# Optimization experiments

Measured on AMD Instinct MI355X. Metric: run time of the kernel, lower is better.

## Reference

```python
import jax, jax.numpy as jnp
import numpy as np

PATCH = 7
PAD = PATCH // 2  # 3


def _to_gray(x):
    # x: [B,3,H,W] -> [B,1,H,W]
    return 0.299 * x[:, 0:1] + 0.587 * x[:, 1:2] + 0.114 * x[:, 2:3]


def _census_transform(x):
    # x: [B,C,H,W] RGB -> grayscale, then 48 shifted binary comparisons.
    if x.shape[1] == 3:
        x = _to_gray(x)
    B, C, H, W = x.shape
    x_pad = jnp.pad(x, ((0, 0), (0, 0), (PAD, PAD), (PAD, PAD)), mode='reflect')
    center = x
    feats = []
    for i in range(PATCH):
        for j in range(PATCH):
            if i == PAD and j == PAD:
                continue
            neighbor = x_pad[:, :, i:i + H, j:j + W]
            feats.append((center > neighbor).astype(x.dtype))
    return jnp.concatenate(feats, axis=1)  # [B,48,H,W]


def setup_inputs() -> dict:
    key = jax.random.key(0)
    k1, k2 = jax.random.split(key)
    B, C, H, W = 8, 3, 512, 512
    pred = jax.random.uniform(k1, (B, C, H, W), dtype=jnp.float32)
    target = jax.random.uniform(k2, (B, C, H, W), dtype=jnp.float32)
    return {"pred": pred, "target": target}


def reference(pred, target):
    pred_census = _census_transform(pred)
    target_census = _census_transform(target)
    return jnp.abs(pred_census - target_census).mean()
```

## Files before the change

kernel.cpp:

```cpp
#include <hip/hip_runtime.h>


#define BATCH 8
#define HH 512
#define WW 512
#define PLANE (HH * WW)
#define TW 64
#define TH 32
#define SCOLS 72
#define HROWS 38
#define KPR 18
#define PITCH 44
#define NT 512
#define LDSZ (SCOLS * PITCH)

__device__ __forceinline__ int refl(int v, int n) {
    return v < 0 ? -v : (v >= n ? 2 * n - 2 - v : v);
}
__device__ __forceinline__ int cbase(int lx) {
    return lx * PITCH + (((lx >> 2) & 7) << 2);
}

__device__ __forceinline__ void load_col10(const float* col, float (&w)[10]) {
    const float4 a = *(const float4*)(col);
    const float4 b = *(const float4*)(col + 4);
    const float2 d = *(const float2*)(col + 8);
    w[0] = a.x; w[1] = a.y; w[2] = a.z; w[3] = a.w;
    w[4] = b.x; w[5] = b.y; w[6] = b.z; w[7] = b.w;
    w[8] = d.x; w[9] = d.y;
}

__global__ __launch_bounds__(NT, 8)
void census_fused(const float* __restrict__ pred,
                  const float* __restrict__ target,
                  float* __restrict__ out) {
    __shared__ __align__(16) float sP[LDSZ];
    __shared__ __align__(16) float sT[LDSZ];

    const int b   = blockIdx.z;
    const int ty0 = blockIdx.y * TH;
    const int tx0 = blockIdx.x * TW;
    const float* __restrict__ pb = pred   + (size_t)b * 3 * PLANE;
    const float* __restrict__ tb = target + (size_t)b * 3 * PLANE;
    const bool fastx = (blockIdx.x >= 1 && blockIdx.x <= 6);

    if (fastx) {
        for (int idx = threadIdx.x; idx < HROWS * KPR; idx += NT) {
            const int hy = idx / KPR;
            const int k  = idx - hy * KPR;
            const int gy  = refl(ty0 + hy - 3, HH);
            const int off = gy * WW + tx0 - 4 + 4 * k;
            const float4 pr = *(const float4*)(pb + off);
            const float4 pg = *(const float4*)(pb + off + PLANE);
            const float4 pc = *(const float4*)(pb + off + 2 * PLANE);
            const float4 tr = *(const float4*)(tb + off);
            const float4 tg = *(const float4*)(tb + off + PLANE);
            const float4 tc = *(const float4*)(tb + off + 2 * PLANE);
            const int lx = 4 * k;
            sP[cbase(lx + 0) + hy] = 0.299f * pr.x + 0.587f * pg.x + 0.114f * pc.x;
            sP[cbase(lx + 1) + hy] = 0.299f * pr.y + 0.587f * pg.y + 0.114f * pc.y;
            sP[cbase(lx + 2) + hy] = 0.299f * pr.z + 0.587f * pg.z + 0.114f * pc.z;
            sP[cbase(lx + 3) + hy] = 0.299f * pr.w + 0.587f * pg.w + 0.114f * pc.w;
            sT[cbase(lx + 0) + hy] = 0.299f * tr.x + 0.587f * tg.x + 0.114f * tc.x;
            sT[cbase(lx + 1) + hy] = 0.299f * tr.y + 0.587f * tg.y + 0.114f * tc.y;
            sT[cbase(lx + 2) + hy] = 0.299f * tr.z + 0.587f * tg.z + 0.114f * tc.z;
            sT[cbase(lx + 3) + hy] = 0.299f * tr.w + 0.587f * tg.w + 0.114f * tc.w;
        }
    } else {
        for (int idx = threadIdx.x; idx < HROWS * SCOLS; idx += NT) {
            const int hy = idx / SCOLS;
            const int lx = idx - hy * SCOLS;
            const int gy  = refl(ty0 + hy - 3, HH);
            const int gx  = refl(tx0 + lx - 4, WW);
            const int off = gy * WW + gx;
            sP[cbase(lx) + hy] = 0.299f * pb[off] + 0.587f * pb[off + PLANE] + 0.114f * pb[off + 2 * PLANE];
            sT[cbase(lx) + hy] = 0.299f * tb[off] + 0.587f * tb[off + PLANE] + 0.114f * tb[off + 2 * PLANE];
        }
    }
    __syncthreads();

    const int wv  = threadIdx.x >> 6;
    const int c   = threadIdx.x & 63;
    const int pr0 = wv * 4;

    float wP[10], wT[10], cP[4], cT[4];
    int cnt = 0;
    load_col10(&sP[cbase(c + 4) + pr0], wP);
    load_col10(&sT[cbase(c + 4) + pr0], wT);
    #pragma unroll
    for (int p = 0; p < 4; ++p) { cP[p] = wP[3 + p]; cT[p] = wT[3 + p]; }
    #pragma unroll
    for (int p = 0; p < 4; ++p) {
        #pragma unroll
        for (int dy = -3; dy <= 3; ++dy) {
            if (dy == 0) continue;
            cnt += ((cP[p] > wP[3 + p + dy]) != (cT[p] > wT[3 + p + dy])) ? 1 : 0;
        }
    }
    #pragma unroll
    for (int t = 0; t < 6; ++t) {
        const int lx = c + 1 + (t < 3 ? t : t + 1);
        load_col10(&sP[cbase(lx) + pr0], wP);
        load_col10(&sT[cbase(lx) + pr0], wT);
        #pragma unroll
        for (int p = 0; p < 4; ++p) {
            #pragma unroll
            for (int dy = -3; dy <= 3; ++dy)
                cnt += ((cP[p] > wP[3 + p + dy]) != (cT[p] > wT[3 + p + dy])) ? 1 : 0;
        }
    }

    #pragma unroll
    for (int o = 32; o > 0; o >>= 1) cnt += __shfl_down(cnt, o, 64);
    __shared__ int wsum[8];
    if ((threadIdx.x & 63) == 0) wsum[wv] = cnt;
    __syncthreads();
    if (threadIdx.x == 0) {
        int tot = 0;
        #pragma unroll
        for (int w = 0; w < 8; ++w) tot += wsum[w];
        atomicAdd(out, (float)tot * (1.0f / 100663296.0f));
    }
}

extern "C" void kernel_launch(void* const* d_in, const int* in_sizes, int n_in,
                              void* d_out, int out_size, void* d_ws, size_t ws_size,
                              hipStream_t stream) {
    const float* pred   = (const float*)d_in[0];
    const float* target = (const float*)d_in[1];
    float* out = (float*)d_out;

    hipMemsetAsync(out, 0, sizeof(float), stream);

    dim3 grid(WW / TW, HH / TH, BATCH);
    census_fused<<<grid, NT, 0, stream>>>(pred, target, out);
}
```

Measured before the change: 100.1 us.

## Process two row tiles per block with double-buffered LDS and register prefetch

Each block now handles two vertically adjacent 64x32 tiles. The global loads for the second tile are issued into registers before the census compare on the first tile runs, so memory latency overlaps with compute, and two LDS buffers are used. Edge columns now go through a reflected gather that builds float4s, replacing the separate scalar path, so all blocks share one loading scheme. The trade-off is double the LDS per block, a lower launch-bounds occupancy hint (4 instead of 8), half as many blocks, and more registers held for the prefetched sets.

```diff
diff --git a/kernel.cpp b/kernel.cpp
--- a/kernel.cpp
+++ b/kernel.cpp
@@ -13,12 +13,62 @@
 #define PITCH 44
 #define NT 512
 #define LDSZ (SCOLS * PITCH)
+#define NSETS (HROWS * KPR)
+#define XSETS (NSETS - NT)
 
 __device__ __forceinline__ int refl(int v, int n) {
     return v < 0 ? -v : (v >= n ? 2 * n - 2 - v : v);
 }
 __device__ __forceinline__ int cbase(int lx) {
     return lx * PITCH + (((lx >> 2) & 7) << 2);
+}
+__device__ __forceinline__ float gray(float r, float g, float b) {
+    return 0.299f * r + 0.587f * g + 0.114f * b;
+}
+
+struct Set6 { float4 pr, pg, pc, tr, tg, tc; };
+
+__device__ __forceinline__ void prefetch_set(const float* __restrict__ pb,
+                                             const float* __restrict__ tb,
+                                             int ty0, int tx0, int sidx, Set6& s) {
+    const int hy  = sidx / KPR;
+    const int k   = sidx - hy * KPR;
+    const int gy  = refl(ty0 + hy - 3, HH);
+    const int gx0 = tx0 - 4 + 4 * k;
+    if (gx0 >= 0 && gx0 <= WW - 4) {
+        const int off = gy * WW + gx0;
+        s.pr = *(const float4*)(pb + off);
+        s.pg = *(const float4*)(pb + off + PLANE);
+        s.pc = *(const float4*)(pb + off + 2 * PLANE);
+        s.tr = *(const float4*)(tb + off);
+        s.tg = *(const float4*)(tb + off + PLANE);
+        s.tc = *(const float4*)(tb + off + 2 * PLANE);
+    } else {
+        const int g0 = (gx0 < 0) ? 4 : 510;
+        const int ro = gy * WW + g0;
+        s.pr = make_float4(pb[ro], pb[ro - 1], pb[ro - 2], pb[ro - 3]);
+        s.pg = make_float4(pb[ro + PLANE], pb[ro - 1 + PLANE], pb[ro - 2 + PLANE], pb[ro - 3 + PLANE]);
+        s.pc = make_float4(pb[ro + 2 * PLANE], pb[ro - 1 + 2 * PLANE], pb[ro - 2 + 2 * PLANE], pb[ro - 3 + 2 * PLANE]);
+        s.tr = make_float4(tb[ro], tb[ro - 1], tb[ro - 2], tb[ro - 3]);
+        s.tg = make_float4(tb[ro + PLANE], tb[ro - 1 + PLANE], tb[ro - 2 + PLANE], tb[ro - 3 + PLANE]);
+        s.tc = make_float4(tb[ro + 2 * PLANE], tb[ro - 1 + 2 * PLANE], tb[ro - 2 + 2 * PLANE], tb[ro - 3 + 2 * PLANE]);
+    }
+}
+
+__device__ __forceinline__ void write_set(float* __restrict__ sP,
+                                          float* __restrict__ sT,
+                                          int sidx, const Set6& s) {
+    const int hy = sidx / KPR;
+    const int k  = sidx - hy * KPR;
+    const int cb = cbase(4 * k) + hy;
+    sP[cb + 0 * PITCH] = gray(s.pr.x, s.pg.x, s.pc.x);
+    sP[cb + 1 * PITCH] = gray(s.pr.y, s.pg.y, s.pc.y);
+    sP[cb + 2 * PITCH] = gray(s.pr.z, s.pg.z, s.pc.z);
+    sP[cb + 3 * PITCH] = gray(s.pr.w, s.pg.w, s.pc.w);
+    sT[cb + 0 * PITCH] = gray(s.tr.x, s.tg.x, s.tc.x);
+    sT[cb + 1 * PITCH] = gray(s.tr.y, s.tg.y, s.tc.y);
+    sT[cb + 2 * PITCH] = gray(s.tr.z, s.tg.z, s.tc.z);
+    sT[cb + 3 * PITCH] = gray(s.tr.w, s.tg.w, s.tc.w);
 }
 
 __device__ __forceinline__ void load_col10(const float* col, float (&w)[10]) {
@@ -30,55 +80,8 @@
     w[8] = d.x; w[9] = d.y;
 }
 
-__global__ __launch_bounds__(NT, 8)
-void census_fused(const float* __restrict__ pred,
-                  const float* __restrict__ target,
-                  float* __restrict__ out) {
-    __shared__ __align__(16) float sP[LDSZ];
-    __shared__ __align__(16) float sT[LDSZ];
-
-    const int b   = blockIdx.z;
-    const int ty0 = blockIdx.y * TH;
-    const int tx0 = blockIdx.x * TW;
-    const float* __restrict__ pb = pred   + (size_t)b * 3 * PLANE;
-    const float* __restrict__ tb = target + (size_t)b * 3 * PLANE;
-    const bool fastx = (blockIdx.x >= 1 && blockIdx.x <= 6);
-
-    if (fastx) {
-        for (int idx = threadIdx.x; idx < HROWS * KPR; idx += NT) {
-            const int hy = idx / KPR;
-            const int k  = idx - hy * KPR;
-            const int gy  = refl(ty0 + hy - 3, HH);
-            const int off = gy * WW + tx0 - 4 + 4 * k;
-            const float4 pr = *(const float4*)(pb + off);
-            const float4 pg = *(const float4*)(pb + off + PLANE);
-            const float4 pc = *(const float4*)(pb + off + 2 * PLANE);
-            const float4 tr = *(const float4*)(tb + off);
-            const float4 tg = *(const float4*)(tb + off + PLANE);
-            const float4 tc = *(const float4*)(tb + off + 2 * PLANE);
-            const int lx = 4 * k;
-            sP[cbase(lx + 0) + hy] = 0.299f * pr.x + 0.587f * pg.x + 0.114f * pc.x;
-            sP[cbase(lx + 1) + hy] = 0.299f * pr.y + 0.587f * pg.y + 0.114f * pc.y;
-            sP[cbase(lx + 2) + hy] = 0.299f * pr.z + 0.587f * pg.z + 0.114f * pc.z;
-            sP[cbase(lx + 3) + hy] = 0.299f * pr.w + 0.587f * pg.w + 0.114f * pc.w;
-            sT[cbase(lx + 0) + hy] = 0.299f * tr.x + 0.587f * tg.x + 0.114f * tc.x;
-            sT[cbase(lx + 1) + hy] = 0.299f * tr.y + 0.587f * tg.y + 0.114f * tc.y;
-            sT[cbase(lx + 2) + hy] = 0.299f * tr.z + 0.587f * tg.z + 0.114f * tc.z;
-            sT[cbase(lx + 3) + hy] = 0.299f * tr.w + 0.587f * tg.w + 0.114f * tc.w;
-        }
-    } else {
-        for (int idx = threadIdx.x; idx < HROWS * SCOLS; idx += NT) {
-            const int hy = idx / SCOLS;
-            const int lx = idx - hy * SCOLS;
-            const int gy  = refl(ty0 + hy - 3, HH);
-            const int gx  = refl(tx0 + lx - 4, WW);
-            const int off = gy * WW + gx;
-            sP[cbase(lx) + hy] = 0.299f * pb[off] + 0.587f * pb[off + PLANE] + 0.114f * pb[off + 2 * PLANE];
-            sT[cbase(lx) + hy] = 0.299f * tb[off] + 0.587f * tb[off + PLANE] + 0.114f * tb[off + 2 * PLANE];
-        }
-    }
-    __syncthreads();
-
+__device__ __forceinline__ int compute_tile(const float* __restrict__ sP,
+                                            const float* __restrict__ sT) {
     const int wv  = threadIdx.x >> 6;
     const int c   = threadIdx.x & 63;
     const int pr0 = wv * 4;
@@ -109,10 +112,48 @@
                 cnt += ((cP[p] > wP[3 + p + dy]) != (cT[p] > wT[3 + p + dy])) ? 1 : 0;
         }
     }
+    return cnt;
+}
+
+__global__ __launch_bounds__(NT, 4)
+void census_fused(const float* __restrict__ pred,
+                  const float* __restrict__ target,
+                  float* __restrict__ out) {
+    __shared__ __align__(16) float sP0[LDSZ];
+    __shared__ __align__(16) float sT0[LDSZ];
+    __shared__ __align__(16) float sP1[LDSZ];
+    __shared__ __align__(16) float sT1[LDSZ];
+
+    const int b    = blockIdx.z;
+    const int tx0  = blockIdx.x * TW;
+    const int ty0A = (blockIdx.y * 2 + 0) * TH;
+    const int ty0B = (blockIdx.y * 2 + 1) * TH;
+    const float* __restrict__ pb = pred   + (size_t)b * 3 * PLANE;
+    const float* __restrict__ tb = target + (size_t)b * 3 * PLANE;
+    const int  tid = threadIdx.x;
+    const bool h1  = tid < XSETS;
+
+    Set6 a0, a1;
+
+    prefetch_set(pb, tb, ty0A, tx0, tid, a0);
+    if (h1) prefetch_set(pb, tb, ty0A, tx0, tid + NT, a1);
+    write_set(sP0, sT0, tid, a0);
+    if (h1) write_set(sP0, sT0, tid + NT, a1);
+    __syncthreads();
+
+    prefetch_set(pb, tb, ty0B, tx0, tid, a0);
+    if (h1) prefetch_set(pb, tb, ty0B, tx0, tid + NT, a1);
+    int cnt = compute_tile(sP0, sT0);
+    write_set(sP1, sT1, tid, a0);
+    if (h1) write_set(sP1, sT1, tid + NT, a1);
+    __syncthreads();
+
+    cnt += compute_tile(sP1, sT1);
 
     #pragma unroll
     for (int o = 32; o > 0; o >>= 1) cnt += __shfl_down(cnt, o, 64);
     __shared__ int wsum[8];
+    const int wv = threadIdx.x >> 6;
     if ((threadIdx.x & 63) == 0) wsum[wv] = cnt;
     __syncthreads();
     if (threadIdx.x == 0) {
@@ -132,6 +173,6 @@
 
     hipMemsetAsync(out, 0, sizeof(float), stream);
 
-    dim3 grid(WW / TW, HH / TH, BATCH);
+    dim3 grid(WW / TW, HH / (2 * TH), BATCH);
     census_fused<<<grid, NT, 0, stream>>>(pred, target, out);
 }
```

Measured after the change: 127.1 us. 1.27x slower.

## Process two row tiles per block with register-prefetched second tile overlapping compute

Applied to the files above, without the earlier changes.

Each block now handles two vertically adjacent 32-row tiles using double LDS buffers. The global loads for the second tile are issued into registers before computing the first tile, so memory latency overlaps with the census comparisons. The grid height is halved and launch bounds are relaxed to 4 blocks per CU to fit the doubled shared memory, which costs occupancy. The edge-column path is restructured into 4-wide groups.

```diff
diff --git a/kernel.cpp b/kernel.cpp
--- a/kernel.cpp
+++ b/kernel.cpp
@@ -13,12 +13,53 @@
 #define PITCH 44
 #define NT 512
 #define LDSZ (SCOLS * PITCH)
+#define NSETS (HROWS * KPR)
+#define XSETS (NSETS - NT)
 
 __device__ __forceinline__ int refl(int v, int n) {
     return v < 0 ? -v : (v >= n ? 2 * n - 2 - v : v);
 }
 __device__ __forceinline__ int cbase(int lx) {
     return lx * PITCH + (((lx >> 2) & 7) << 2);
+}
+__device__ __forceinline__ float gray(float r, float g, float b) {
+    return 0.299f * r + 0.587f * g + 0.114f * b;
+}
+
+__device__ __forceinline__ void stage_set(const float* __restrict__ pb,
+                                          const float* __restrict__ tb,
+                                          int ty0, int tx0, int sidx,
+                                          float* __restrict__ sP,
+                                          float* __restrict__ sT, bool fast) {
+    const int hy = sidx / KPR;
+    const int k  = sidx - hy * KPR;
+    const int gy = refl(ty0 + hy - 3, HH);
+    const int cb = cbase(4 * k) + hy;
+    if (fast) {
+        const int off = gy * WW + tx0 - 4 + 4 * k;
+        const float4 pr = *(const float4*)(pb + off);
+        const float4 pg = *(const float4*)(pb + off + PLANE);
+        const float4 pc = *(const float4*)(pb + off + 2 * PLANE);
+        const float4 tr = *(const float4*)(tb + off);
+        const float4 tg = *(const float4*)(tb + off + PLANE);
+        const float4 tc = *(const float4*)(tb + off + 2 * PLANE);
+        sP[cb + 0 * PITCH] = gray(pr.x, pg.x, pc.x);
+        sP[cb + 1 * PITCH] = gray(pr.y, pg.y, pc.y);
+        sP[cb + 2 * PITCH] = gray(pr.z, pg.z, pc.z);
+        sP[cb + 3 * PITCH] = gray(pr.w, pg.w, pc.w);
+        sT[cb + 0 * PITCH] = gray(tr.x, tg.x, tc.x);
+        sT[cb + 1 * PITCH] = gray(tr.y, tg.y, tc.y);
+        sT[cb + 2 * PITCH] = gray(tr.z, tg.z, tc.z);
+        sT[cb + 3 * PITCH] = gray(tr.w, tg.w, tc.w);
+    } else {
+        #pragma unroll
+        for (int i = 0; i < 4; ++i) {
+            const int gx  = refl(tx0 - 4 + 4 * k + i, WW);
+            const int off = gy * WW + gx;
+            sP[cb + i * PITCH] = gray(pb[off], pb[off + PLANE], pb[off + 2 * PLANE]);
+            sT[cb + i * PITCH] = gray(tb[off], tb[off + PLANE], tb[off + 2 * PLANE]);
+        }
+    }
 }
 
 __device__ __forceinline__ void load_col10(const float* col, float (&w)[10]) {
@@ -30,55 +71,8 @@
     w[8] = d.x; w[9] = d.y;
 }
 
-__global__ __launch_bounds__(NT, 8)
-void census_fused(const float* __restrict__ pred,
-                  const float* __restrict__ target,
-                  float* __restrict__ out) {
-    __shared__ __align__(16) float sP[LDSZ];
-    __shared__ __align__(16) float sT[LDSZ];
-
-    const int b   = blockIdx.z;
-    const int ty0 = blockIdx.y * TH;
-    const int tx0 = blockIdx.x * TW;
-    const float* __restrict__ pb = pred   + (size_t)b * 3 * PLANE;
-    const float* __restrict__ tb = target + (size_t)b * 3 * PLANE;
-    const bool fastx = (blockIdx.x >= 1 && blockIdx.x <= 6);
-
-    if (fastx) {
-        for (int idx = threadIdx.x; idx < HROWS * KPR; idx += NT) {
-            const int hy = idx / KPR;
-            const int k  = idx - hy * KPR;
-            const int gy  = refl(ty0 + hy - 3, HH);
-            const int off = gy * WW + tx0 - 4 + 4 * k;
-            const float4 pr = *(const float4*)(pb + off);
-            const float4 pg = *(const float4*)(pb + off + PLANE);
-            const float4 pc = *(const float4*)(pb + off + 2 * PLANE);
-            const float4 tr = *(const float4*)(tb + off);
-            const float4 tg = *(const float4*)(tb + off + PLANE);
-            const float4 tc = *(const float4*)(tb + off + 2 * PLANE);
-            const int lx = 4 * k;
-            sP[cbase(lx + 0) + hy] = 0.299f * pr.x + 0.587f * pg.x + 0.114f * pc.x;
-            sP[cbase(lx + 1) + hy] = 0.299f * pr.y + 0.587f * pg.y + 0.114f * pc.y;
-            sP[cbase(lx + 2) + hy] = 0.299f * pr.z + 0.587f * pg.z + 0.114f * pc.z;
-            sP[cbase(lx + 3) + hy] = 0.299f * pr.w + 0.587f * pg.w + 0.114f * pc.w;
-            sT[cbase(lx + 0) + hy] = 0.299f * tr.x + 0.587f * tg.x + 0.114f * tc.x;
-            sT[cbase(lx + 1) + hy] = 0.299f * tr.y + 0.587f * tg.y + 0.114f * tc.y;
-            sT[cbase(lx + 2) + hy] = 0.299f * tr.z + 0.587f * tg.z + 0.114f * tc.z;
-            sT[cbase(lx + 3) + hy] = 0.299f * tr.w + 0.587f * tg.w + 0.114f * tc.w;
-        }
-    } else {
-        for (int idx = threadIdx.x; idx < HROWS * SCOLS; idx += NT) {
-            const int hy = idx / SCOLS;
-            const int lx = idx - hy * SCOLS;
-            const int gy  = refl(ty0 + hy - 3, HH);
-            const int gx  = refl(tx0 + lx - 4, WW);
-            const int off = gy * WW + gx;
-            sP[cbase(lx) + hy] = 0.299f * pb[off] + 0.587f * pb[off + PLANE] + 0.114f * pb[off + 2 * PLANE];
-            sT[cbase(lx) + hy] = 0.299f * tb[off] + 0.587f * tb[off + PLANE] + 0.114f * tb[off + 2 * PLANE];
-        }
-    }
-    __syncthreads();
-
+__device__ __forceinline__ int compute_tile(const float* __restrict__ sP,
+                                            const float* __restrict__ sT) {
     const int wv  = threadIdx.x >> 6;
     const int c   = threadIdx.x & 63;
     const int pr0 = wv * 4;
@@ -109,10 +103,81 @@
                 cnt += ((cP[p] > wP[3 + p + dy]) != (cT[p] > wT[3 + p + dy])) ? 1 : 0;
         }
     }
+    return cnt;
+}
+
+__global__ __launch_bounds__(NT, 4)
+void census_fused(const float* __restrict__ pred,
+                  const float* __restrict__ target,
+                  float* __restrict__ out) {
+    __shared__ __align__(16) float sP0[LDSZ];
+    __shared__ __align__(16) float sT0[LDSZ];
+    __shared__ __align__(16) float sP1[LDSZ];
+    __shared__ __align__(16) float sT1[LDSZ];
+
+    const int b    = blockIdx.z;
+    const int tx0  = blockIdx.x * TW;
+    const int ty0A = (blockIdx.y * 2 + 0) * TH;
+    const int ty0B = (blockIdx.y * 2 + 1) * TH;
+    const float* __restrict__ pb = pred   + (size_t)b * 3 * PLANE;
+    const float* __restrict__ tb = target + (size_t)b * 3 * PLANE;
+    const int  tid  = threadIdx.x;
+    const bool fastx = (blockIdx.x >= 1 && blockIdx.x <= 6);
+
+    for (int idx = tid; idx < NSETS; idx += NT)
+        stage_set(pb, tb, ty0A, tx0, idx, sP0, sT0, fastx);
+    __syncthreads();
+
+    float4 pr, pg, pc, tr, tg, tc;
+    int pcb;
+    {
+        const int hy = tid / KPR;
+        const int k  = tid - hy * KPR;
+        const int gy = refl(ty0B + hy - 3, HH);
+        pcb = cbase(4 * k) + hy;
+        if (fastx) {
+            const int off = gy * WW + tx0 - 4 + 4 * k;
+            pr = *(const float4*)(pb + off);
+            pg = *(const float4*)(pb + off + PLANE);
+            pc = *(const float4*)(pb + off + 2 * PLANE);
+            tr = *(const float4*)(tb + off);
+            tg = *(const float4*)(tb + off + PLANE);
+            tc = *(const float4*)(tb + off + 2 * PLANE);
+        } else {
+            const int o0 = gy * WW + refl(tx0 - 4 + 4 * k + 0, WW);
+            const int o1 = gy * WW + refl(tx0 - 4 + 4 * k + 1, WW);
+            const int o2 = gy * WW + refl(tx0 - 4 + 4 * k + 2, WW);
+            const int o3 = gy * WW + refl(tx0 - 4 + 4 * k + 3, WW);
+            pr = make_float4(pb[o0], pb[o1], pb[o2], pb[o3]);
+            pg = make_float4(pb[o0 + PLANE], pb[o1 + PLANE], pb[o2 + PLANE], pb[o3 + PLANE]);
+            pc = make_float4(pb[o0 + 2 * PLANE], pb[o1 + 2 * PLANE], pb[o2 + 2 * PLANE], pb[o3 + 2 * PLANE]);
+            tr = make_float4(tb[o0], tb[o1], tb[o2], tb[o3]);
+            tg = make_float4(tb[o0 + PLANE], tb[o1 + PLANE], tb[o2 + PLANE], tb[o3 + PLANE]);
+            tc = make_float4(tb[o0 + 2 * PLANE], tb[o1 + 2 * PLANE], tb[o2 + 2 * PLANE], tb[o3 + 2 * PLANE]);
+        }
+    }
+    __builtin_amdgcn_sched_barrier(0);
+
+    int cnt = compute_tile(sP0, sT0);
+
+    sP1[pcb + 0 * PITCH] = gray(pr.x, pg.x, pc.x);
+    sP1[pcb + 1 * PITCH] = gray(pr.y, pg.y, pc.y);
+    sP1[pcb + 2 * PITCH] = gray(pr.z, pg.z, pc.z);
+    sP1[pcb + 3 * PITCH] = gray(pr.w, pg.w, pc.w);
+    sT1[pcb + 0 * PITCH] = gray(tr.x, tg.x, tc.x);
+    sT1[pcb + 1 * PITCH] = gray(tr.y, tg.y, tc.y);
+    sT1[pcb + 2 * PITCH] = gray(tr.z, tg.z, tc.z);
+    sT1[pcb + 3 * PITCH] = gray(tr.w, tg.w, tc.w);
+    if (tid < XSETS)
+        stage_set(pb, tb, ty0B, tx0, tid + NT, sP1, sT1, fastx);
+    __syncthreads();
+
+    cnt += compute_tile(sP1, sT1);
 
     #pragma unroll
     for (int o = 32; o > 0; o >>= 1) cnt += __shfl_down(cnt, o, 64);
     __shared__ int wsum[8];
+    const int wv = threadIdx.x >> 6;
     if ((threadIdx.x & 63) == 0) wsum[wv] = cnt;
     __syncthreads();
     if (threadIdx.x == 0) {
@@ -132,6 +197,6 @@
 
     hipMemsetAsync(out, 0, sizeof(float), stream);
 
-    dim3 grid(WW / TW, HH / TH, BATCH);
+    dim3 grid(WW / TW, HH / (2 * TH), BATCH);
     census_fused<<<grid, NT, 0, stream>>>(pred, target, out);
 }
```

Result: slower. 123.6 us (+23.5%).
